# Optimization experiments

Hardware: AMD Instinct MI355X
Metric: run time of the kernel (lower is better)

Reference implementation:

```python
import jax, jax.numpy as jnp
import numpy as np

B, N_DET, N_T, NY, NX = 8, 128, 2048, 256, 256


def setup_inputs() -> dict:
    key = jax.random.key(0)
    k1, k2, k3 = jax.random.split(key, 3)
    sino = jax.random.normal(k1, (B, 1, N_DET, N_T), dtype=jnp.float32)
    # LUT channel 0: fractional time index (some out-of-range to exercise valid mask)
    lut0 = jax.random.uniform(k2, (NY, NX, N_DET), dtype=jnp.float32,
                              minval=-8.0, maxval=float(N_T) + 8.0)
    alpha = jax.random.uniform(k3, (NY, NX, N_DET), dtype=jnp.float32)
    k_floor = jnp.floor(lut0)
    valid = (k_floor >= 0) & (k_floor < N_T - 1)
    k0 = jnp.clip(k_floor, 0, N_T - 2).astype(jnp.int32)
    # Hann apodization window over detectors
    win = 0.5 - 0.5 * np.cos(2.0 * np.pi * np.arange(N_DET) / max(N_DET - 1, 1))
    apod = jnp.asarray(win.astype(np.float32))
    return {"sino": sino, "alpha": alpha, "apod": apod, "k0": k0, "valid": valid}


def reference(sino, alpha, apod, k0, valid):
    # Per-sample normalization over (n_det, n_t)
    eps = jnp.finfo(sino.dtype).eps
    mean = jnp.mean(sino, axis=(-1, -2), keepdims=True)
    centered = sino - mean
    std = jnp.sqrt(jnp.mean(centered * centered, axis=(-1, -2), keepdims=True) + eps)
    S = (centered / std)[:, 0]                     # [B, n_det, n_t]

    P = NY * NX
    kd = jnp.transpose(k0, (2, 0, 1)).reshape(N_DET, P)      # [n_det, P]
    ad = jnp.transpose(alpha, (2, 0, 1)).reshape(N_DET, P)   # [n_det, P]
    vd = jnp.transpose(valid, (2, 0, 1)).reshape(N_DET, P).astype(S.dtype)

    idx0 = jnp.broadcast_to(kd[None], (B, N_DET, P))
    s0 = jnp.take_along_axis(S, idx0, axis=2)                # [B, n_det, P]
    s1 = jnp.take_along_axis(S, idx0 + 1, axis=2)            # [B, n_det, P]
    sk = ((1.0 - ad) * s0 + ad * s1) * vd                    # linear interp + mask

    out = jnp.einsum('d,bdp->bp', apod, sk).reshape(B, NY, NX)
    norm = jnp.maximum(jnp.sum(apod), jnp.finfo(apod.dtype).tiny)
    return (out / norm)[:, None]                             # [B, 1, ny, nx]
```

## Files before the change

### kernel.cpp

```cpp
#include <hip/hip_runtime.h>
#include <hip/hip_fp16.h>

#define NB    8
#define NDET  128
#define NT    2048
#define NPIX  65536
#define NELEM (NDET * NT)
#define NGRP  32


#define WS_S16_OFF   8192
#define WS_PT_OFF    (8192 + (size_t)NDET * NT * NB * 2)
#define WS3_REQUIRED (WS_PT_OFF + (size_t)NGRP * NPIX * NB * 2)
#define WS2_REQUIRED (WS_PT_OFF + (size_t)8 * NB * NPIX * 4)

__global__ __launch_bounds__(256) void k_stats(const float* __restrict__ sino,
                                               double* __restrict__ wsd) {
    const int bx = blockIdx.x;
    const int b = bx >> 5, i = bx & 31;
    const float4* src = (const float4*)(sino + (size_t)b * NELEM);
    const int base = i * 2048;
    double s = 0.0, ss = 0.0;
    for (int r = 0; r < 8; ++r) {
        float4 v = src[base + r * 256 + threadIdx.x];
        double d0 = v.x, d1 = v.y, d2 = v.z, d3 = v.w;
        s  += d0 + d1 + d2 + d3;
        ss += d0 * d0 + d1 * d1 + d2 * d2 + d3 * d3;
    }
    for (int off = 32; off; off >>= 1) {
        s  += __shfl_down(s, off);
        ss += __shfl_down(ss, off);
    }
    __shared__ double lds[8];
    const int wave = threadIdx.x >> 6;
    if ((threadIdx.x & 63) == 0) { lds[wave * 2] = s; lds[wave * 2 + 1] = ss; }
    __syncthreads();
    if (threadIdx.x == 0) {
        double S = 0, SS = 0;
        for (int w = 0; w < 4; ++w) { S += lds[w * 2]; SS += lds[w * 2 + 1]; }
        wsd[bx * 2] = S; wsd[bx * 2 + 1] = SS;
    }
}

__global__ __launch_bounds__(256) void k_finalize(const float* __restrict__ apod,
                                                  const unsigned char* __restrict__ validb,
                                                  const double* __restrict__ wsd,
                                                  float* __restrict__ wsf) {
    __shared__ float sap[NDET];
    __shared__ int sflag;
    const int t = threadIdx.x;
    if (t == 0) sflag = 0;
    if (t < NDET) sap[t] = apod[t];
    int local = 0;
    {
        const unsigned char* vb = validb + t * 256;
        for (int j = 1; j < 256; j += 4) local |= (vb[j] != 0);
    }
    __syncthreads();
    if (local) atomicOr(&sflag, 1);
    if (t < NB) {
        double S = 0, SS = 0;
        for (int i = 0; i < 32; ++i) {
            S  += wsd[(t * 32 + i) * 2];
            SS += wsd[(t * 32 + i) * 2 + 1];
        }
        double mean = S / (double)NELEM;
        double var  = SS / (double)NELEM - mean * mean;
        double istd = 1.0 / sqrt(var + (double)(1.1920928955078125e-07f));
        wsf[t]     = (float)mean;
        wsf[8 + t] = (float)istd;
    }
    if (t == 0) {
        double a = 0;
        for (int d = 0; d < NDET; ++d) a += (double)sap[d];
        float norm = fmaxf((float)a, 1.1754943508222875e-38f);
        wsf[17] = 1.0f / norm;
    }
    __syncthreads();
    if (t < NDET) wsf[32 + t] = sap[t] * wsf[17];
    if (t == 0) ((unsigned int*)wsf)[16] = (unsigned int)(sflag != 0);
}

__global__ __launch_bounds__(256) void k_build(const float* __restrict__ sino,
                                               const float* __restrict__ wsf,
                                               __half* __restrict__ S16) {
    const int dt = blockIdx.x * 256 + threadIdx.x;
    union { uint4 q; __half h[8]; } u;
#pragma unroll
    for (int b = 0; b < NB; ++b) {
        float x = sino[(size_t)b * NELEM + dt];
        u.h[b] = __float2half((x - wsf[b]) * wsf[8 + b]);
    }
    *(uint4*)(S16 + (size_t)dt * 8) = u.q;
}

__device__ __forceinline__ float2 h2f(unsigned int w) {
    __half2 h;
    *reinterpret_cast<unsigned int*>(&h) = w;
    return __half22float2(h);
}

__global__ __launch_bounds__(1024) void k_das5(const int* __restrict__ k0,
                                               const float* __restrict__ alpha,
                                               const void* __restrict__ valid,
                                               const __half* __restrict__ S16,
                                               const float* __restrict__ wsf,
                                               __half* __restrict__ pT) {
    __shared__ __align__(16) __half SL[4 * NT * NB];
    const int x     = blockIdx.x & 7;
    const int sub   = (blockIdx.x >> 3) & 3;
    const int chunk = blockIdx.x >> 5;
    const int g     = x * 4 + sub;
    {
        const uint4* src = (const uint4*)(S16 + (size_t)g * 4 * NT * NB);
        uint4* dst = (uint4*)SL;
#pragma unroll
        for (int i = 0; i < 8; ++i)
            dst[i * 1024 + threadIdx.x] = src[i * 1024 + threadIdx.x];
    }
    __syncthreads();

    const unsigned int mode = ((const unsigned int*)wsf)[16];
    float apn[4];
#pragma unroll
    for (int j = 0; j < 4; ++j) apn[j] = wsf[32 + g * 4 + j];

    const int p0 = chunk * 8192 + (int)threadIdx.x;
    size_t li = (size_t)p0 * NDET + g * 4;

    int4         kb = *(const int4*)(k0 + li);
    float4       ab = *(const float4*)(alpha + li);
    unsigned int vB = 0;
    uint4        vW = {0u, 0u, 0u, 0u};
    if (mode) vB = *(const unsigned int*)((const unsigned char*)valid + li);
    else      vW = *(const uint4*)((const unsigned int*)valid + li);

    for (int it = 0; it < 8; ++it) {
        const int4         kc = kb;
        const float4       ac = ab;
        const unsigned int cB = vB;
        const uint4        cW = vW;
        if (it < 7) {
            const size_t lin = li + (size_t)1024 * NDET;
            kb = *(const int4*)(k0 + lin);
            ab = *(const float4*)(alpha + lin);
            if (mode) vB = *(const unsigned int*)((const unsigned char*)valid + lin);
            else      vW = *(const uint4*)((const unsigned int*)valid + lin);
        }
        unsigned int vbits;
        if (mode)
            vbits = ((cB & 0xffu) ? 1u : 0u) | ((cB & 0xff00u) ? 2u : 0u) |
                    ((cB & 0xff0000u) ? 4u : 0u) | ((cB & 0xff000000u) ? 8u : 0u);
        else
            vbits = (cW.x ? 1u : 0u) | (cW.y ? 2u : 0u) | (cW.z ? 4u : 0u) | (cW.w ? 8u : 0u);

        const int   kk[4] = {kc.x, kc.y, kc.z, kc.w};
        const float aa[4] = {ac.x, ac.y, ac.z, ac.w};
        float acc[NB] = {0.f, 0.f, 0.f, 0.f, 0.f, 0.f, 0.f, 0.f};
#pragma unroll
        for (int j = 0; j < 4; ++j) {
            const float w  = ((vbits >> j) & 1u) ? apn[j] : 0.0f;
            const float wb = w * aa[j];
            const float wa = w - wb;
            const uint4* s = (const uint4*)(SL + ((size_t)(j * NT + kk[j]) << 3));
            uint4 q0 = s[0];
            uint4 q1 = s[1];
            const unsigned int w0[4] = {q0.x, q0.y, q0.z, q0.w};
            const unsigned int w1[4] = {q1.x, q1.y, q1.z, q1.w};
#pragma unroll
            for (int h = 0; h < 4; ++h) {
                float2 f0 = h2f(w0[h]);
                float2 f1 = h2f(w1[h]);
                acc[2 * h]     += wa * f0.x + wb * f1.x;
                acc[2 * h + 1] += wa * f0.y + wb * f1.y;
            }
        }
        union { uint4 q; __half2 h[4]; } o;
#pragma unroll
        for (int h = 0; h < 4; ++h)
            o.h[h] = __floats2half2_rn(acc[2 * h], acc[2 * h + 1]);
        const int p = p0 + it * 1024;
        *(uint4*)(pT + ((size_t)g * NPIX + p) * NB) = o.q;
        li += (size_t)1024 * NDET;
    }
}

__global__ __launch_bounds__(256) void k_reduce2(const __half* __restrict__ pT,
                                                 float* __restrict__ out) {
    const int p = blockIdx.x * 256 + threadIdx.x;
    float acc[NB] = {0.f, 0.f, 0.f, 0.f, 0.f, 0.f, 0.f, 0.f};
#pragma unroll
    for (int g = 0; g < NGRP; ++g) {
        union { uint4 q; __half2 h[4]; } u;
        u.q = *(const uint4*)(pT + ((size_t)g * NPIX + p) * NB);
#pragma unroll
        for (int h = 0; h < 4; ++h) {
            float2 f = __half22float2(u.h[h]);
            acc[2 * h]     += f.x;
            acc[2 * h + 1] += f.y;
        }
    }
#pragma unroll
    for (int b = 0; b < NB; ++b)
        out[(size_t)b * NPIX + p] = acc[b];
}

__global__ __launch_bounds__(1024) void k_das2(const int* __restrict__ k0,
                                               const float* __restrict__ alpha,
                                               const void* __restrict__ valid,
                                               const __half* __restrict__ S16,
                                               const float* __restrict__ wsf,
                                               float* __restrict__ partials) {
    const int px = threadIdx.x & 255;
    const int dc = threadIdx.x >> 8;
    const int slice = blockIdx.x & 7;
    const int chunk = blockIdx.x >> 3;
    const int p  = chunk * 256 + px;
    const int d0 = slice * 16 + dc * 4;
    const unsigned int mode = ((const unsigned int*)wsf)[16];
    const float* apodn = wsf + 32;

    float acc[NB] = {0.f, 0.f, 0.f, 0.f, 0.f, 0.f, 0.f, 0.f};
    const size_t lbase = (size_t)p * NDET + d0;

    int4   k4 = *(const int4*)(k0 + lbase);
    float4 a4 = *(const float4*)(alpha + lbase);
    unsigned int vbits;
    if (mode) {
        unsigned int v4 = *(const unsigned int*)((const unsigned char*)valid + lbase);
        vbits = ((v4 & 0xffu) ? 1u : 0u) | (((v4 >> 8) & 0xffu) ? 2u : 0u) |
                (((v4 >> 16) & 0xffu) ? 4u : 0u) | ((v4 >> 24) ? 8u : 0u);
    } else {
        uint4 v4 = *(const uint4*)((const unsigned int*)valid + lbase);
        vbits = (v4.x ? 1u : 0u) | (v4.y ? 2u : 0u) | (v4.z ? 4u : 0u) | (v4.w ? 8u : 0u);
    }
    const int   kk[4] = {k4.x, k4.y, k4.z, k4.w};
    const float aa[4] = {a4.x, a4.y, a4.z, a4.w};
#pragma unroll
    for (int j = 0; j < 4; ++j) {
        const int d = d0 + j;
        const float w  = ((vbits >> j) & 1u) ? apodn[d] : 0.0f;
        const float wb = w * aa[j];
        const float wa = w - wb;
        const uint4* s = (const uint4*)(S16 + ((size_t)(d * NT + kk[j]) << 3));
        uint4 q0 = s[0];
        uint4 q1 = s[1];
        const unsigned int w0[4] = {q0.x, q0.y, q0.z, q0.w};
        const unsigned int w1[4] = {q1.x, q1.y, q1.z, q1.w};
#pragma unroll
        for (int h = 0; h < 4; ++h) {
            float2 f0 = h2f(w0[h]);
            float2 f1 = h2f(w1[h]);
            acc[2 * h]     += wa * f0.x + wb * f1.x;
            acc[2 * h + 1] += wa * f0.y + wb * f1.y;
        }
    }

    __shared__ float red[1024][9];
#pragma unroll
    for (int b = 0; b < NB; ++b) red[threadIdx.x][b] = acc[b];
    __syncthreads();
    if (dc == 0) {
#pragma unroll
        for (int b = 0; b < NB; ++b) {
            float v = red[px][b] + red[px + 256][b] + red[px + 512][b] + red[px + 768][b];
            partials[((size_t)slice * NB + b) * NPIX + p] = v;
        }
    }
}

__global__ __launch_bounds__(256) void k_reduce(const float* __restrict__ partials,
                                                float* __restrict__ out) {
    const int i = (blockIdx.x * 256 + threadIdx.x) * 4;
    float4 s = {0.f, 0.f, 0.f, 0.f};
#pragma unroll
    for (int g = 0; g < 8; ++g) {
        float4 v = *(const float4*)(partials + (size_t)g * NB * NPIX + i);
        s.x += v.x; s.y += v.y; s.z += v.z; s.w += v.w;
    }
    *(float4*)(out + i) = s;
}

extern "C" void kernel_launch(void* const* d_in, const int* in_sizes, int n_in,
                              void* d_out, int out_size, void* d_ws, size_t ws_size,
                              hipStream_t stream) {
    const float* sino  = (const float*)d_in[0];
    const float* alpha = (const float*)d_in[1];
    const float* apod  = (const float*)d_in[2];
    const int*   k0    = (const int*)d_in[3];
    const void*  valid = d_in[4];

    float*  out = (float*)d_out;
    double* wsd = (double*)d_ws;
    float*  wsf = (float*)((char*)d_ws + 4096);
    __half* S16 = (__half*)((char*)d_ws + WS_S16_OFF);
    __half* pT  = (__half*)((char*)d_ws + WS_PT_OFF);
    float*  parts = (float*)((char*)d_ws + WS_PT_OFF);

    k_stats   <<<256,  256, 0, stream>>>(sino, wsd);
    k_finalize<<<1,    256, 0, stream>>>(apod, (const unsigned char*)valid, wsd, wsf);
    k_build   <<<1024, 256, 0, stream>>>(sino, wsf, S16);
    if (ws_size >= WS3_REQUIRED) {
        k_das5   <<<256, 1024, 0, stream>>>(k0, alpha, valid, S16, wsf, pT);
        k_reduce2<<<256,  256, 0, stream>>>(pT, out);
    } else {
        k_das2  <<<2048, 1024, 0, stream>>>(k0, alpha, valid, S16, wsf, parts);
        k_reduce<<<512,   256, 0, stream>>>(parts, out);
    }
}
```

Baseline: 72.73 us.

## Pack k0/alpha/valid into per-group 32-bit words before the DAS gather kernel

Adds a k_pack kernel that transposes the per-pixel LUT data (k0, alpha, valid) into a group-major layout. Each detector entry becomes one 32-bit word: an 11-bit index, a valid bit and alpha stored as fp16. The DAS kernel then reads one coalesced uint4 per pixel per group and writes its fp16 partial sums in place over the packed buffer. The aim is to replace strided 16-byte loads from three arrays with contiguous loads. The cost is an extra full pass over the LUT inputs every call, and alpha is quantised to fp16.

```diff
diff --git a/kernel.cpp b/kernel.cpp
--- a/kernel.cpp
+++ b/kernel.cpp
@@ -11,7 +11,7 @@
 
 #define WS_S16_OFF   8192
 #define WS_PT_OFF    (8192 + (size_t)NDET * NT * NB * 2)
-#define WS3_REQUIRED (WS_PT_OFF + (size_t)NGRP * NPIX * NB * 2)
+#define WS7_REQUIRED (WS_PT_OFF + (size_t)NGRP * NPIX * NB * 2)
 #define WS2_REQUIRED (WS_PT_OFF + (size_t)8 * NB * NPIX * 4)
 
 __global__ __launch_bounds__(256) void k_stats(const float* __restrict__ sino,
@@ -94,18 +94,62 @@
     *(uint4*)(S16 + (size_t)dt * 8) = u.q;
 }
 
+__global__ __launch_bounds__(256) void k_pack(const int* __restrict__ k0,
+                                              const float* __restrict__ alpha,
+                                              const void* __restrict__ valid,
+                                              const float* __restrict__ wsf,
+                                              uint4* __restrict__ packT) {
+    __shared__ uint4 T[NGRP][65];
+    const unsigned int mode = ((const unsigned int*)wsf)[16];
+    const int tile = blockIdx.x;
+    const size_t eb = (size_t)tile * 64 * NDET;
+    const int t = threadIdx.x;
+#pragma unroll
+    for (int i = 0; i < 8; ++i) {
+        const int flat = t + i * 256;
+        const int px = flat >> 5, q = flat & 31;
+        int4   kq = *(const int4*)(k0 + eb + (size_t)flat * 4);
+        float4 aq = *(const float4*)(alpha + eb + (size_t)flat * 4);
+        unsigned int vb[4];
+        if (mode) {
+            unsigned int v = *(const unsigned int*)((const unsigned char*)valid + eb + (size_t)flat * 4);
+            vb[0] = v & 0xffu; vb[1] = (v >> 8) & 0xffu;
+            vb[2] = (v >> 16) & 0xffu; vb[3] = v >> 24;
+        } else {
+            uint4 v = *(const uint4*)((const unsigned int*)valid + eb + (size_t)flat * 4);
+            vb[0] = v.x; vb[1] = v.y; vb[2] = v.z; vb[3] = v.w;
+        }
+        const int   ks[4] = {kq.x, kq.y, kq.z, kq.w};
+        const float as[4] = {aq.x, aq.y, aq.z, aq.w};
+        uint4 o;
+        unsigned int* ow = (unsigned int*)&o;
+#pragma unroll
+        for (int j = 0; j < 4; ++j) {
+            __half ha = __float2half_rn(as[j]);
+            unsigned short hb = *(unsigned short*)&ha;
+            ow[j] = ((unsigned int)ks[j] & 0x7FFu) | ((vb[j] ? 1u : 0u) << 11) |
+                    ((unsigned int)hb << 16);
+        }
+        T[q][px] = o;
+    }
+    __syncthreads();
+    const int g = t >> 3, si = t & 7;
+#pragma unroll
+    for (int r = 0; r < 8; ++r) {
+        const int pxl = si + r * 8;
+        packT[(size_t)g * NPIX + tile * 64 + pxl] = T[g][pxl];
+    }
+}
+
 __device__ __forceinline__ float2 h2f(unsigned int w) {
     __half2 h;
     *reinterpret_cast<unsigned int*>(&h) = w;
     return __half22float2(h);
 }
 
-__global__ __launch_bounds__(1024) void k_das5(const int* __restrict__ k0,
-                                               const float* __restrict__ alpha,
-                                               const void* __restrict__ valid,
+__global__ __launch_bounds__(1024) void k_das7(uint4* pk,
                                                const __half* __restrict__ S16,
-                                               const float* __restrict__ wsf,
-                                               __half* __restrict__ pT) {
+                                               const float* __restrict__ wsf) {
     __shared__ __align__(16) __half SL[4 * NT * NB];
     const int x     = blockIdx.x & 7;
     const int sub   = (blockIdx.x >> 3) & 3;
@@ -120,49 +164,30 @@
     }
     __syncthreads();
 
-    const unsigned int mode = ((const unsigned int*)wsf)[16];
     float apn[4];
 #pragma unroll
     for (int j = 0; j < 4; ++j) apn[j] = wsf[32 + g * 4 + j];
 
     const int p0 = chunk * 8192 + (int)threadIdx.x;
-    size_t li = (size_t)p0 * NDET + g * 4;
-
-    int4         kb = *(const int4*)(k0 + li);
-    float4       ab = *(const float4*)(alpha + li);
-    unsigned int vB = 0;
-    uint4        vW = {0u, 0u, 0u, 0u};
-    if (mode) vB = *(const unsigned int*)((const unsigned char*)valid + li);
-    else      vW = *(const uint4*)((const unsigned int*)valid + li);
-
+    const size_t base = (size_t)g * NPIX + p0;
+
+    uint4 pkb = pk[base];
     for (int it = 0; it < 8; ++it) {
-        const int4         kc = kb;
-        const float4       ac = ab;
-        const unsigned int cB = vB;
-        const uint4        cW = vW;
-        if (it < 7) {
-            const size_t lin = li + (size_t)1024 * NDET;
-            kb = *(const int4*)(k0 + lin);
-            ab = *(const float4*)(alpha + lin);
-            if (mode) vB = *(const unsigned int*)((const unsigned char*)valid + lin);
-            else      vW = *(const uint4*)((const unsigned int*)valid + lin);
-        }
-        unsigned int vbits;
-        if (mode)
-            vbits = ((cB & 0xffu) ? 1u : 0u) | ((cB & 0xff00u) ? 2u : 0u) |
-                    ((cB & 0xff0000u) ? 4u : 0u) | ((cB & 0xff000000u) ? 8u : 0u);
-        else
-            vbits = (cW.x ? 1u : 0u) | (cW.y ? 2u : 0u) | (cW.z ? 4u : 0u) | (cW.w ? 8u : 0u);
-
-        const int   kk[4] = {kc.x, kc.y, kc.z, kc.w};
-        const float aa[4] = {ac.x, ac.y, ac.z, ac.w};
+        const uint4 pkc = pkb;
+        if (it < 7) pkb = pk[base + (size_t)(it + 1) * 1024];
+
+        const unsigned int pw[4] = {pkc.x, pkc.y, pkc.z, pkc.w};
         float acc[NB] = {0.f, 0.f, 0.f, 0.f, 0.f, 0.f, 0.f, 0.f};
 #pragma unroll
         for (int j = 0; j < 4; ++j) {
-            const float w  = ((vbits >> j) & 1u) ? apn[j] : 0.0f;
-            const float wb = w * aa[j];
+            const unsigned int wj = pw[j];
+            const int kk = (int)(wj & 0x7FFu);
+            unsigned short hb = (unsigned short)(wj >> 16);
+            const float aa = __half2float(*(const __half*)&hb);
+            const float w  = (wj & 0x800u) ? apn[j] : 0.0f;
+            const float wb = w * aa;
             const float wa = w - wb;
-            const uint4* s = (const uint4*)(SL + ((size_t)(j * NT + kk[j]) << 3));
+            const uint4* s = (const uint4*)(SL + ((size_t)(j * NT + kk) << 3));
             uint4 q0 = s[0];
             uint4 q1 = s[1];
             const unsigned int w0[4] = {q0.x, q0.y, q0.z, q0.w};
@@ -179,9 +204,7 @@
 #pragma unroll
         for (int h = 0; h < 4; ++h)
             o.h[h] = __floats2half2_rn(acc[2 * h], acc[2 * h + 1]);
-        const int p = p0 + it * 1024;
-        *(uint4*)(pT + ((size_t)g * NPIX + p) * NB) = o.q;
-        li += (size_t)1024 * NDET;
+        pk[base + (size_t)it * 1024] = o.q;
     }
 }
 
@@ -294,15 +317,16 @@
     double* wsd = (double*)d_ws;
     float*  wsf = (float*)((char*)d_ws + 4096);
     __half* S16 = (__half*)((char*)d_ws + WS_S16_OFF);
-    __half* pT  = (__half*)((char*)d_ws + WS_PT_OFF);
+    uint4*  pk  = (uint4*)((char*)d_ws + WS_PT_OFF);
     float*  parts = (float*)((char*)d_ws + WS_PT_OFF);
 
     k_stats   <<<256,  256, 0, stream>>>(sino, wsd);
     k_finalize<<<1,    256, 0, stream>>>(apod, (const unsigned char*)valid, wsd, wsf);
     k_build   <<<1024, 256, 0, stream>>>(sino, wsf, S16);
-    if (ws_size >= WS3_REQUIRED) {
-        k_das5   <<<256, 1024, 0, stream>>>(k0, alpha, valid, S16, wsf, pT);
-        k_reduce2<<<256,  256, 0, stream>>>(pT, out);
+    if (ws_size >= WS7_REQUIRED) {
+        k_pack   <<<1024, 256, 0, stream>>>(k0, alpha, valid, wsf, pk);
+        k_das7   <<<256, 1024, 0, stream>>>(pk, S16, wsf);
+        k_reduce2<<<256,  256, 0, stream>>>((const __half*)pk, out);
     } else {
         k_das2  <<<2048, 1024, 0, stream>>>(k0, alpha, valid, S16, wsf, parts);
         k_reduce<<<512,   256, 0, stream>>>(parts, out);
```

Measured after the change: 65.57 us. 9.8% less time.

## Gather sinogram directly from global memory and reduce detector groups via shuffles

Applied to the files above, without the earlier changes.

Replaces the LDS-staged gather kernel with one where each group of four adjacent threads handles four detector groups of one pixel. The threads read the fp16 sinogram straight from global/L2, issue all gathers before doing the math, and combine partial sums with xor-shuffles. Only 8 partial slices per pixel are written instead of 32, which shrinks the partial-buffer traffic and the final reduction work. The LUT loads are marked nontemporal. In exchange, random gathers now hit L2 instead of LDS, which risks higher gather latency.

```diff
diff --git a/kernel.cpp b/kernel.cpp
--- a/kernel.cpp
+++ b/kernel.cpp
@@ -8,11 +8,14 @@
 #define NELEM (NDET * NT)
 #define NGRP  32
 
+typedef int          i32x4 __attribute__((ext_vector_type(4)));
+typedef float        f32x4 __attribute__((ext_vector_type(4)));
+typedef unsigned int u32x4 __attribute__((ext_vector_type(4)));
+
 
 #define WS_S16_OFF   8192
 #define WS_PT_OFF    (8192 + (size_t)NDET * NT * NB * 2)
-#define WS3_REQUIRED (WS_PT_OFF + (size_t)NGRP * NPIX * NB * 2)
-#define WS2_REQUIRED (WS_PT_OFF + (size_t)8 * NB * NPIX * 4)
+#define WS11_REQUIRED (WS_PT_OFF + (size_t)8 * NPIX * NB * 2)
 
 __global__ __launch_bounds__(256) void k_stats(const float* __restrict__ sino,
                                                double* __restrict__ wsd) {
@@ -100,73 +103,74 @@
     return __half22float2(h);
 }
 
-__global__ __launch_bounds__(1024) void k_das5(const int* __restrict__ k0,
-                                               const float* __restrict__ alpha,
-                                               const void* __restrict__ valid,
-                                               const __half* __restrict__ S16,
-                                               const float* __restrict__ wsf,
-                                               __half* __restrict__ pT) {
-    __shared__ __align__(16) __half SL[4 * NT * NB];
-    const int x     = blockIdx.x & 7;
-    const int sub   = (blockIdx.x >> 3) & 3;
-    const int chunk = blockIdx.x >> 5;
-    const int g     = x * 4 + sub;
-    {
-        const uint4* src = (const uint4*)(S16 + (size_t)g * 4 * NT * NB);
-        uint4* dst = (uint4*)SL;
-#pragma unroll
-        for (int i = 0; i < 8; ++i)
-            dst[i * 1024 + threadIdx.x] = src[i * 1024 + threadIdx.x];
-    }
-    __syncthreads();
-
+__global__ __launch_bounds__(256, 4) void k_das11(const int* __restrict__ k0,
+                                                  const float* __restrict__ alpha,
+                                                  const void* __restrict__ valid,
+                                                  const __half* __restrict__ S16,
+                                                  const float* __restrict__ wsf,
+                                                  uint4* __restrict__ pS) {
+    const int x = blockIdx.x & 7;
+    const int c = blockIdx.x >> 3;
+    const int gsub = threadIdx.x & 3;
+    const int pl   = threadIdx.x >> 2;
+    const int g    = x * 4 + gsub;
     const unsigned int mode = ((const unsigned int*)wsf)[16];
     float apn[4];
 #pragma unroll
     for (int j = 0; j < 4; ++j) apn[j] = wsf[32 + g * 4 + j];
 
-    const int p0 = chunk * 8192 + (int)threadIdx.x;
-    size_t li = (size_t)p0 * NDET + g * 4;
-
-    int4         kb = *(const int4*)(k0 + li);
-    float4       ab = *(const float4*)(alpha + li);
-    unsigned int vB = 0;
-    uint4        vW = {0u, 0u, 0u, 0u};
-    if (mode) vB = *(const unsigned int*)((const unsigned char*)valid + li);
-    else      vW = *(const uint4*)((const unsigned int*)valid + li);
-
-    for (int it = 0; it < 8; ++it) {
-        const int4         kc = kb;
-        const float4       ac = ab;
-        const unsigned int cB = vB;
-        const uint4        cW = vW;
-        if (it < 7) {
-            const size_t lin = li + (size_t)1024 * NDET;
-            kb = *(const int4*)(k0 + lin);
-            ab = *(const float4*)(alpha + lin);
-            if (mode) vB = *(const unsigned int*)((const unsigned char*)valid + lin);
-            else      vW = *(const uint4*)((const unsigned int*)valid + lin);
-        }
-        unsigned int vbits;
+    const __half* Sg = S16;
+
+    i32x4 kq; f32x4 aq; unsigned int vq;
+    {
+        const size_t e = ((size_t)(c * 256 + pl) * NDET) + g * 4;
+        kq = __builtin_nontemporal_load((const i32x4*)(k0 + e));
+        aq = __builtin_nontemporal_load((const f32x4*)(alpha + e));
+        if (mode) {
+            vq = __builtin_nontemporal_load((const unsigned int*)((const unsigned char*)valid + e));
+        } else {
+            u32x4 v = __builtin_nontemporal_load((const u32x4*)((const unsigned int*)valid + e));
+            vq = (v.x ? 1u : 0u) | (v.y ? 2u : 0u) | (v.z ? 4u : 0u) | (v.w ? 8u : 0u);
+        }
+    }
+
+    for (int i = 0; i < 4; ++i) {
+        const i32x4        kc = kq;
+        const f32x4        ac = aq;
+        unsigned int       vc = vq;
+        if (i < 3) {
+            const size_t e = ((size_t)(c * 256 + (i + 1) * 64 + pl) * NDET) + g * 4;
+            kq = __builtin_nontemporal_load((const i32x4*)(k0 + e));
+            aq = __builtin_nontemporal_load((const f32x4*)(alpha + e));
+            if (mode) {
+                vq = __builtin_nontemporal_load((const unsigned int*)((const unsigned char*)valid + e));
+            } else {
+                u32x4 v = __builtin_nontemporal_load((const u32x4*)((const unsigned int*)valid + e));
+                vq = (v.x ? 1u : 0u) | (v.y ? 2u : 0u) | (v.z ? 4u : 0u) | (v.w ? 8u : 0u);
+            }
+        }
         if (mode)
-            vbits = ((cB & 0xffu) ? 1u : 0u) | ((cB & 0xff00u) ? 2u : 0u) |
-                    ((cB & 0xff0000u) ? 4u : 0u) | ((cB & 0xff000000u) ? 8u : 0u);
-        else
-            vbits = (cW.x ? 1u : 0u) | (cW.y ? 2u : 0u) | (cW.z ? 4u : 0u) | (cW.w ? 8u : 0u);
+            vc = ((vc & 0xffu) ? 1u : 0u) | ((vc & 0xff00u) ? 2u : 0u) |
+                 ((vc & 0xff0000u) ? 4u : 0u) | ((vc & 0xff000000u) ? 8u : 0u);
 
         const int   kk[4] = {kc.x, kc.y, kc.z, kc.w};
         const float aa[4] = {ac.x, ac.y, ac.z, ac.w};
+        uint4 q0[4], q1[4];
+#pragma unroll
+        for (int j = 0; j < 4; ++j) {
+            const int d = g * 4 + j;
+            const uint4* s = (const uint4*)(Sg + ((size_t)(d * NT + kk[j]) << 3));
+            q0[j] = s[0];
+            q1[j] = s[1];
+        }
         float acc[NB] = {0.f, 0.f, 0.f, 0.f, 0.f, 0.f, 0.f, 0.f};
 #pragma unroll
         for (int j = 0; j < 4; ++j) {
-            const float w  = ((vbits >> j) & 1u) ? apn[j] : 0.0f;
+            const float w  = ((vc >> j) & 1u) ? apn[j] : 0.0f;
             const float wb = w * aa[j];
             const float wa = w - wb;
-            const uint4* s = (const uint4*)(SL + ((size_t)(j * NT + kk[j]) << 3));
-            uint4 q0 = s[0];
-            uint4 q1 = s[1];
-            const unsigned int w0[4] = {q0.x, q0.y, q0.z, q0.w};
-            const unsigned int w1[4] = {q1.x, q1.y, q1.z, q1.w};
+            const unsigned int w0[4] = {q0[j].x, q0[j].y, q0[j].z, q0[j].w};
+            const unsigned int w1[4] = {q1[j].x, q1[j].y, q1[j].z, q1[j].w};
 #pragma unroll
             for (int h = 0; h < 4; ++h) {
                 float2 f0 = h2f(w0[h]);
@@ -175,24 +179,30 @@
                 acc[2 * h + 1] += wa * f0.y + wb * f1.y;
             }
         }
-        union { uint4 q; __half2 h[4]; } o;
-#pragma unroll
-        for (int h = 0; h < 4; ++h)
-            o.h[h] = __floats2half2_rn(acc[2 * h], acc[2 * h + 1]);
-        const int p = p0 + it * 1024;
-        *(uint4*)(pT + ((size_t)g * NPIX + p) * NB) = o.q;
-        li += (size_t)1024 * NDET;
-    }
-}
-
-__global__ __launch_bounds__(256) void k_reduce2(const __half* __restrict__ pT,
+#pragma unroll
+        for (int b = 0; b < NB; ++b) {
+            acc[b] += __shfl_xor(acc[b], 1);
+            acc[b] += __shfl_xor(acc[b], 2);
+        }
+        if (gsub == 0) {
+            union { uint4 q; __half2 h[4]; } o;
+#pragma unroll
+            for (int h = 0; h < 4; ++h)
+                o.h[h] = __floats2half2_rn(acc[2 * h], acc[2 * h + 1]);
+            const int p = c * 256 + i * 64 + pl;
+            pS[(size_t)x * NPIX + p] = o.q;
+        }
+    }
+}
+
+__global__ __launch_bounds__(256) void k_reduce3(const uint4* __restrict__ pS,
                                                  float* __restrict__ out) {
     const int p = blockIdx.x * 256 + threadIdx.x;
     float acc[NB] = {0.f, 0.f, 0.f, 0.f, 0.f, 0.f, 0.f, 0.f};
 #pragma unroll
-    for (int g = 0; g < NGRP; ++g) {
+    for (int x = 0; x < 8; ++x) {
         union { uint4 q; __half2 h[4]; } u;
-        u.q = *(const uint4*)(pT + ((size_t)g * NPIX + p) * NB);
+        u.q = pS[(size_t)x * NPIX + p];
 #pragma unroll
         for (int h = 0; h < 4; ++h) {
             float2 f = __half22float2(u.h[h]);
@@ -294,15 +304,15 @@
     double* wsd = (double*)d_ws;
     float*  wsf = (float*)((char*)d_ws + 4096);
     __half* S16 = (__half*)((char*)d_ws + WS_S16_OFF);
-    __half* pT  = (__half*)((char*)d_ws + WS_PT_OFF);
+    uint4*  pS  = (uint4*)((char*)d_ws + WS_PT_OFF);
     float*  parts = (float*)((char*)d_ws + WS_PT_OFF);
 
     k_stats   <<<256,  256, 0, stream>>>(sino, wsd);
     k_finalize<<<1,    256, 0, stream>>>(apod, (const unsigned char*)valid, wsd, wsf);
     k_build   <<<1024, 256, 0, stream>>>(sino, wsf, S16);
-    if (ws_size >= WS3_REQUIRED) {
-        k_das5   <<<256, 1024, 0, stream>>>(k0, alpha, valid, S16, wsf, pT);
-        k_reduce2<<<256,  256, 0, stream>>>(pT, out);
+    if (ws_size >= WS11_REQUIRED) {
+        k_das11  <<<2048, 256, 0, stream>>>(k0, alpha, valid, S16, wsf, pS);
+        k_reduce3<<<256,  256, 0, stream>>>(pS, out);
     } else {
         k_das2  <<<2048, 1024, 0, stream>>>(k0, alpha, valid, S16, wsf, parts);
         k_reduce<<<512,   256, 0, stream>>>(parts, out);
```

Measured after the change: 102.8 us. 1.41x slower.

## Coalesce LUT loads via cooperative wave loads and shuffle redistribution

Applied to the files above, without the earlier changes.

In the main gather kernel, each wave now loads the per-pixel k0, alpha and valid entries so that neighbouring lanes read adjacent 16-byte chunks of a pixel's detector row, instead of each thread reading a strided 16-byte slice. The values are then redistributed to the owning lanes with cross-lane shuffles and selects. The partial-sum buffer is re-laid out as 64-pixel tiles with the group index interleaved, and the reduce kernel is updated to match. This is meant to cut uncoalesced global traffic on the large LUT reads, at the cost of many extra shuffle instructions and more registers for the four prefetched sets.

```diff
diff --git a/kernel.cpp b/kernel.cpp
--- a/kernel.cpp
+++ b/kernel.cpp
@@ -11,8 +11,7 @@
 
 #define WS_S16_OFF   8192
 #define WS_PT_OFF    (8192 + (size_t)NDET * NT * NB * 2)
-#define WS3_REQUIRED (WS_PT_OFF + (size_t)NGRP * NPIX * NB * 2)
-#define WS2_REQUIRED (WS_PT_OFF + (size_t)8 * NB * NPIX * 4)
+#define WS13_REQUIRED (WS_PT_OFF + (size_t)NGRP * NPIX * NB * 2)
 
 __global__ __launch_bounds__(256) void k_stats(const float* __restrict__ sino,
                                                double* __restrict__ wsd) {
@@ -100,12 +99,19 @@
     return __half22float2(h);
 }
 
-__global__ __launch_bounds__(1024) void k_das5(const int* __restrict__ k0,
-                                               const float* __restrict__ alpha,
-                                               const void* __restrict__ valid,
-                                               const __half* __restrict__ S16,
-                                               const float* __restrict__ wsf,
-                                               __half* __restrict__ pT) {
+__device__ __forceinline__ int   pick4i(int a, int b, int c, int d, int j) {
+    int ra = (j & 1) ? b : a, rb = (j & 1) ? d : c; return (j & 2) ? rb : ra;
+}
+__device__ __forceinline__ float pick4f(float a, float b, float c, float d, int j) {
+    float ra = (j & 1) ? b : a, rb = (j & 1) ? d : c; return (j & 2) ? rb : ra;
+}
+
+__global__ __launch_bounds__(1024) void k_das13(const int* __restrict__ k0,
+                                                const float* __restrict__ alpha,
+                                                const void* __restrict__ valid,
+                                                const __half* __restrict__ S16,
+                                                const float* __restrict__ wsf,
+                                                uint4* __restrict__ pT) {
     __shared__ __align__(16) __half SL[4 * NT * NB];
     const int x     = blockIdx.x & 7;
     const int sub   = (blockIdx.x >> 3) & 3;
@@ -125,43 +131,72 @@
 #pragma unroll
     for (int j = 0; j < 4; ++j) apn[j] = wsf[32 + g * 4 + j];
 
-    const int p0 = chunk * 8192 + (int)threadIdx.x;
-    size_t li = (size_t)p0 * NDET + g * 4;
-
-    int4         kb = *(const int4*)(k0 + li);
-    float4       ab = *(const float4*)(alpha + li);
-    unsigned int vB = 0;
-    uint4        vW = {0u, 0u, 0u, 0u};
-    if (mode) vB = *(const unsigned int*)((const unsigned char*)valid + li);
-    else      vW = *(const uint4*)((const unsigned int*)valid + li);
-
+    const int tid  = (int)threadIdx.x;
+    const int w    = tid >> 6;
+    const int lane = tid & 63;
+    const int q    = lane & 3;
+    const int pxo  = lane >> 2;
+    const int srcl = ((lane & 15) << 2) | sub;
+    const int jsel = lane >> 4;
+    const int pw   = chunk * 8192 + w * 512;
+    const int ebase = x * 16 + q * 4;
+
+    int4 kn[4]; float4 an[4]; unsigned int vn[4];
+#define LOADSETS(IT)                                                          \
+    {                                                                         \
+        _Pragma("unroll")                                                     \
+        for (int j = 0; j < 4; ++j) {                                         \
+            const size_t e = (size_t)(pw + (IT) * 64 + j * 16 + pxo) * NDET + ebase; \
+            kn[j] = *(const int4*)(k0 + e);                                   \
+            an[j] = *(const float4*)(alpha + e);                              \
+            if (mode) {                                                       \
+                vn[j] = *(const unsigned int*)((const unsigned char*)valid + e); \
+            } else {                                                          \
+                uint4 v = *(const uint4*)((const unsigned int*)valid + e);    \
+                vn[j] = (v.x ? 1u : 0u) | (v.y ? 2u : 0u) |                   \
+                        (v.z ? 4u : 0u) | (v.w ? 8u : 0u);                    \
+            }                                                                 \
+        }                                                                     \
+    }
+
+    LOADSETS(0)
     for (int it = 0; it < 8; ++it) {
-        const int4         kc = kb;
-        const float4       ac = ab;
-        const unsigned int cB = vB;
-        const uint4        cW = vW;
-        if (it < 7) {
-            const size_t lin = li + (size_t)1024 * NDET;
-            kb = *(const int4*)(k0 + lin);
-            ab = *(const float4*)(alpha + lin);
-            if (mode) vB = *(const unsigned int*)((const unsigned char*)valid + lin);
-            else      vW = *(const uint4*)((const unsigned int*)valid + lin);
-        }
-        unsigned int vbits;
-        if (mode)
-            vbits = ((cB & 0xffu) ? 1u : 0u) | ((cB & 0xff00u) ? 2u : 0u) |
-                    ((cB & 0xff0000u) ? 4u : 0u) | ((cB & 0xff000000u) ? 8u : 0u);
-        else
-            vbits = (cW.x ? 1u : 0u) | (cW.y ? 2u : 0u) | (cW.z ? 4u : 0u) | (cW.w ? 8u : 0u);
-
-        const int   kk[4] = {kc.x, kc.y, kc.z, kc.w};
-        const float aa[4] = {ac.x, ac.y, ac.z, ac.w};
+        int4 kc[4]; float4 ac[4]; unsigned int vc[4];
+#pragma unroll
+        for (int j = 0; j < 4; ++j) { kc[j] = kn[j]; ac[j] = an[j]; vc[j] = vn[j]; }
+        if (it < 7) LOADSETS(it + 1)
+
+        int kk[4]; float aa[4]; unsigned int vb;
+#pragma unroll
+        for (int cmp = 0; cmp < 4; ++cmp) {
+            int t0 = __shfl(((const int*)&kc[0])[cmp], srcl);
+            int t1 = __shfl(((const int*)&kc[1])[cmp], srcl);
+            int t2 = __shfl(((const int*)&kc[2])[cmp], srcl);
+            int t3 = __shfl(((const int*)&kc[3])[cmp], srcl);
+            kk[cmp] = pick4i(t0, t1, t2, t3, jsel);
+            float f0 = __shfl(((const float*)&ac[0])[cmp], srcl);
+            float f1 = __shfl(((const float*)&ac[1])[cmp], srcl);
+            float f2 = __shfl(((const float*)&ac[2])[cmp], srcl);
+            float f3 = __shfl(((const float*)&ac[3])[cmp], srcl);
+            aa[cmp] = pick4f(f0, f1, f2, f3, jsel);
+        }
+        {
+            int t0 = __shfl((int)vc[0], srcl);
+            int t1 = __shfl((int)vc[1], srcl);
+            int t2 = __shfl((int)vc[2], srcl);
+            int t3 = __shfl((int)vc[3], srcl);
+            unsigned int vr = (unsigned int)pick4i(t0, t1, t2, t3, jsel);
+            vb = mode ? (((vr & 0xffu) ? 1u : 0u) | ((vr & 0xff00u) ? 2u : 0u) |
+                         ((vr & 0xff0000u) ? 4u : 0u) | ((vr & 0xff000000u) ? 8u : 0u))
+                      : vr;
+        }
+
         float acc[NB] = {0.f, 0.f, 0.f, 0.f, 0.f, 0.f, 0.f, 0.f};
 #pragma unroll
         for (int j = 0; j < 4; ++j) {
-            const float w  = ((vbits >> j) & 1u) ? apn[j] : 0.0f;
-            const float wb = w * aa[j];
-            const float wa = w - wb;
+            const float wgt = ((vb >> j) & 1u) ? apn[j] : 0.0f;
+            const float wb  = wgt * aa[j];
+            const float wa  = wgt - wb;
             const uint4* s = (const uint4*)(SL + ((size_t)(j * NT + kk[j]) << 3));
             uint4 q0 = s[0];
             uint4 q1 = s[1];
@@ -175,24 +210,26 @@
                 acc[2 * h + 1] += wa * f0.y + wb * f1.y;
             }
         }
-        union { uint4 q; __half2 h[4]; } o;
+        union { uint4 qq; __half2 h[4]; } o;
 #pragma unroll
         for (int h = 0; h < 4; ++h)
             o.h[h] = __floats2half2_rn(acc[2 * h], acc[2 * h + 1]);
-        const int p = p0 + it * 1024;
-        *(uint4*)(pT + ((size_t)g * NPIX + p) * NB) = o.q;
-        li += (size_t)1024 * NDET;
-    }
+        const int p = pw + it * 64 + lane;
+        pT[(size_t)(p >> 6) * 2048 + g * 64 + (p & 63)] = o.qq;
+    }
+#undef LOADSETS
 }
 
 __global__ __launch_bounds__(256) void k_reduce2(const __half* __restrict__ pT,
                                                  float* __restrict__ out) {
     const int p = blockIdx.x * 256 + threadIdx.x;
+    const int tile = p >> 6, pl = p & 63;
+    const uint4* pq = (const uint4*)pT;
     float acc[NB] = {0.f, 0.f, 0.f, 0.f, 0.f, 0.f, 0.f, 0.f};
 #pragma unroll
     for (int g = 0; g < NGRP; ++g) {
         union { uint4 q; __half2 h[4]; } u;
-        u.q = *(const uint4*)(pT + ((size_t)g * NPIX + p) * NB);
+        u.q = pq[(size_t)tile * 2048 + g * 64 + pl];
 #pragma unroll
         for (int h = 0; h < 4; ++h) {
             float2 f = __half22float2(u.h[h]);
@@ -294,15 +331,15 @@
     double* wsd = (double*)d_ws;
     float*  wsf = (float*)((char*)d_ws + 4096);
     __half* S16 = (__half*)((char*)d_ws + WS_S16_OFF);
-    __half* pT  = (__half*)((char*)d_ws + WS_PT_OFF);
+    uint4*  pT  = (uint4*)((char*)d_ws + WS_PT_OFF);
     float*  parts = (float*)((char*)d_ws + WS_PT_OFF);
 
     k_stats   <<<256,  256, 0, stream>>>(sino, wsd);
     k_finalize<<<1,    256, 0, stream>>>(apod, (const unsigned char*)valid, wsd, wsf);
     k_build   <<<1024, 256, 0, stream>>>(sino, wsf, S16);
-    if (ws_size >= WS3_REQUIRED) {
-        k_das5   <<<256, 1024, 0, stream>>>(k0, alpha, valid, S16, wsf, pT);
-        k_reduce2<<<256,  256, 0, stream>>>(pT, out);
+    if (ws_size >= WS13_REQUIRED) {
+        k_das13  <<<256, 1024, 0, stream>>>(k0, alpha, valid, S16, wsf, pT);
+        k_reduce2<<<256,  256, 0, stream>>>((const __half*)pT, out);
     } else {
         k_das2  <<<2048, 1024, 0, stream>>>(k0, alpha, valid, S16, wsf, parts);
         k_reduce<<<512,   256, 0, stream>>>(parts, out);
```

After: 76.65 us. 5.4% more time.
